# Optimization experiments

Measured on AMD Instinct MI355X. Metric: run time of the kernel, lower is better.

## Reference

```python
import jax, jax.numpy as jnp
import numpy as np

ALPHA = 0.3      # keras LeakyReLU default
BN_EPS = 1e-3    # keras BatchNormalization default
RF, STRIDE = 8, 8


def leaky(x):
    return jnp.where(x >= 0, x, ALPHA * x)


def batchnorm(x, gamma, beta):
    # training-mode BN (train_flag=True): batch statistics over N,H,W
    mean = jnp.mean(x, axis=(0, 1, 2), keepdims=True)
    var = jnp.var(x, axis=(0, 1, 2), keepdims=True)
    return gamma * (x - mean) * jax.lax.rsqrt(var + BN_EPS) + beta


def cbl(x, W, gamma, beta):
    y = jax.lax.conv_general_dilated(x, W, (1, 1), 'SAME',
                                     dimension_numbers=('NHWC', 'HWIO', 'NHWC'))
    return leaky(batchnorm(y, gamma, beta))


def tcbl(x, W, gamma, beta):
    y = jax.lax.conv_transpose(x, W, (2, 2), 'SAME',
                               dimension_numbers=('NHWC', 'HWIO', 'NHWC'))
    return leaky(batchnorm(y, gamma, beta))


def setup_inputs() -> dict:
    key = jax.random.key(0)
    ks = jax.random.split(key, 8)
    B, H, W, C = 8, 128, 128, 128
    nH = (H - RF) // STRIDE + 1
    nW = (W - RF) // STRIDE + 1
    nWin = nH * nW  # 256
    inputs = jax.random.normal(ks[0], (B, H, W, C), dtype=jnp.float32)
    conv_scale = 1.0 / np.sqrt(3 * 3 * C)
    Wq = jax.random.normal(ks[1], (3, 3, C, 128), dtype=jnp.float32) * conv_scale
    Wk = jax.random.normal(ks[2], (3, 3, C, 128), dtype=jnp.float32) * conv_scale
    beta_bias = jax.random.normal(ks[3], (1, 1, 1, nWin), dtype=jnp.float32) * 0.05
    Wt = jax.random.normal(ks[4], (4, 4, nWin, 128), dtype=jnp.float32) / np.sqrt(4 * 4 * nWin)
    return {
        'inputs': inputs,
        'Wq': Wq, 'gq': jnp.ones((128,), jnp.float32), 'bq': jnp.zeros((128,), jnp.float32),
        'Wk': Wk, 'gk': jnp.ones((128,), jnp.float32), 'bk': jnp.zeros((128,), jnp.float32),
        'beta_bias': beta_bias,
        'g1': jnp.ones((nWin,), jnp.float32), 'b1': jnp.zeros((nWin,), jnp.float32),
        'Wt': Wt, 'gt': jnp.ones((128,), jnp.float32), 'bt': jnp.zeros((128,), jnp.float32),
    }


def reference(inputs, Wq, gq, bq, Wk, gk, bk, beta_bias, g1, b1, Wt, gt, bt):
    Q = cbl(inputs, Wq, gq, bq)   # (B,H,W,C)
    K = cbl(inputs, Wk, gk, bk)
    B, H, W, C = Q.shape
    nH = (H - RF) // STRIDE + 1
    nW = (W - RF) // STRIDE + 1
    # window start indices -> (n, RF) gather index grids
    hh = (jnp.arange(nH) * STRIDE)[:, None] + jnp.arange(RF)[None, :]
    ww = (jnp.arange(nW) * STRIDE)[:, None] + jnp.arange(RF)[None, :]

    def patches(x):
        # (B, nH, nW, RF, RF, C) -> (B, nWin, RF*RF*C)
        p = x[:, hh[:, None, :, None], ww[None, :, None, :], :]
        return p.reshape(B, nH * nW, RF * RF * C)

    Qp = patches(Q)
    Kp = patches(K)
    # sim[b, f, q] = <K window f, Q window q>; collapses the 4-nested loop
    sim = jnp.einsum('bfd,bqd->bfq', Kp, Qp).reshape(B, nH, nW, nH * nW)
    sim = sim + beta_bias
    act = leaky(batchnorm(sim, g1, b1))
    return tcbl(act, Wt, gt, bt)  # (B, 2*nH, 2*nW, 128)
```

## Files before the change

### kernel.cpp

```cpp
#include <hip/hip_runtime.h>

typedef __attribute__((ext_vector_type(8))) short bf16x8;
typedef __attribute__((ext_vector_type(8))) unsigned short u16x8;
typedef __attribute__((ext_vector_type(4))) float f32x4;

__device__ __forceinline__ unsigned short f2b(float x) {
    unsigned int u = __float_as_uint(x);
    u += 0x7FFFu + ((u >> 16) & 1u);
    return (unsigned short)(u >> 16);
}
__device__ __forceinline__ float b2f(unsigned short h) {
    return __uint_as_float(((unsigned int)h) << 16);
}
__device__ __forceinline__ float lrelu(float v) { return v >= 0.f ? v : 0.3f * v; }

#define GLL(gp, lp) __builtin_amdgcn_global_load_lds( \
    (const __attribute__((address_space(1))) unsigned int*)(gp), \
    (__attribute__((address_space(3))) unsigned int*)(lp), 16, 0, 0)


__global__ __launch_bounds__(256) void k0a_prep(
        const float* __restrict__ Wq, const float* __restrict__ Wk,
        const float* __restrict__ Wt, unsigned short* __restrict__ WqT,
        unsigned short* __restrict__ WkT, unsigned short* __restrict__ WtT,
        float* __restrict__ S) {
    int idx = blockIdx.x * 256 + threadIdx.x;
    int gs = gridDim.x * 256;
    for (int i = idx; i < 2048; i += gs) S[i] = 0.f;
    for (int i = idx; i < 147456; i += gs) {
        int tap = i >> 14, r = i & 16383, ci = r >> 7, co = r & 127;
        int ch = ci >> 6, e = ci & 63;
        int dst = ((tap * 2 + ch) * 128 + co) * 64 + (((e >> 3) ^ (co & 7)) << 3) + (e & 7);
        WqT[dst] = f2b(Wq[i]);
        WkT[dst] = f2b(Wk[i]);
    }
    for (int i = idx; i < 524288; i += gs) {
        int t = i >> 15, r = i & 32767, ci = r >> 7, co = r & 127;
        WtT[(((size_t)t << 7) + co) * 256 + ci] = f2b(Wt[i]);
    }
}

__global__ __launch_bounds__(256) void k0b_padx(const float* __restrict__ X,
                                                unsigned short* __restrict__ Xb) {
    int c = blockIdx.x * 256 + threadIdx.x;
    int k8 = c & 7;
    int t = c >> 3;
    int wp = t % 130; t /= 130;
    int ch = t & 1; t >>= 1;
    int hp = t % 130; int b = t / 130;
    u16x8 o;
    if (hp >= 1 && hp <= 128 && wp >= 1 && wp <= 128) {
        const float* s = X + (((size_t)(b * 128 + hp - 1) * 128) + (wp - 1)) * 128 + ch * 64 + k8 * 8;
        float4 f0 = *(const float4*)(s);
        float4 f1 = *(const float4*)(s + 4);
        o[0] = f2b(f0.x); o[1] = f2b(f0.y); o[2] = f2b(f0.z); o[3] = f2b(f0.w);
        o[4] = f2b(f1.x); o[5] = f2b(f1.y); o[6] = f2b(f1.z); o[7] = f2b(f1.w);
    } else {
#pragma unroll
        for (int j = 0; j < 8; ++j) o[j] = 0;
    }
    *(u16x8*)&Xb[(size_t)c * 8] = o;
}

__global__ __launch_bounds__(512, 4) void k1_conv(
        const unsigned short* __restrict__ Xb,
        const unsigned short* __restrict__ WqT, const unsigned short* __restrict__ WkT,
        unsigned short* __restrict__ Qraw, unsigned short* __restrict__ Kraw,
        float* __restrict__ S) {
    __shared__ unsigned short s_row[2 * 130 * 72];
    __shared__ unsigned short s_w[2][128 * 64];
    __shared__ float s_st[256];
    const int tid = threadIdx.x;
    const int x = blockIdx.x;
    const int xcd = x & 7, sdec = x >> 3;
    const int b = sdec >> 4, r16 = sdec & 15;
    const int hp = xcd * 8 + (r16 >> 1), conv = r16 & 1;
    const int h0 = hp * 2;
    const int lane = tid & 63, wv = tid >> 6;
    const int wm = wv & 3, wn = wv >> 2;
    const int l15 = lane & 15, kof = (lane >> 4) * 8;
    const int ar = wm >> 1;
    const int awb = (wm & 1) * 64;
    const int nb = wn * 64;

    const unsigned short* W = conv ? WkT : WqT;
    const int gofs = wv * 2048 + lane * 16;

    f32x4 acc[4][4];
#pragma unroll
    for (int i = 0; i < 4; ++i)
#pragma unroll
        for (int j = 0; j < 4; ++j) acc[i][j] = (f32x4){0.f, 0.f, 0.f, 0.f};
    if (tid < 256) s_st[tid] = 0.f;

    {
        const char* src = (const char*)W;
        char* dst = (char*)&s_w[0][0] + wv * 2048;
        GLL(src + gofs, dst);
        GLL(src + gofs + 1024, dst + 1024);
    }

#pragma unroll
    for (int ch = 0; ch < 2; ++ch) {
#pragma unroll
        for (int dy = 0; dy < 3; ++dy) {
#pragma unroll
            for (int dx = 0; dx < 3; ++dx) {
                const int p = (ch * 3 + dy) * 3 + dx;
                __builtin_amdgcn_s_barrier();
                if (dx == 0) {
                    const unsigned short* src0 = Xb + (size_t)((b * 130 + h0 + dy) * 2 + ch) * 8320;
                    const unsigned short* src1 = Xb + (size_t)((b * 130 + h0 + dy + 1) * 2 + ch) * 8320;
                    for (int c = tid; c < 2080; c += 512) {
                        int r = (c >= 1040);
                        int cw = r ? c - 1040 : c;
                        int w = cw >> 3, k8 = cw & 7;
                        *(u16x8*)&s_row[(r * 130 + w) * 72 + k8 * 8] =
                            *(const u16x8*)&((r ? src1 : src0)[cw * 8]);
                    }
                }
                if (p < 17) {
                    const int pn = p + 1;
                    const int nch = pn / 9, ntap = pn % 9;
                    const char* src = (const char*)(W + ((size_t)(ntap * 2 + nch) << 13));
                    char* dst = (char*)&s_w[pn & 1][0] + wv * 2048;
                    GLL(src + gofs, dst);
                    GLL(src + gofs + 1024, dst + 1024);
                    asm volatile("s_waitcnt vmcnt(2) lgkmcnt(0)" ::: "memory");
                } else {
                    asm volatile("s_waitcnt vmcnt(0) lgkmcnt(0)" ::: "memory");
                }
                __builtin_amdgcn_sched_barrier(0);
                __builtin_amdgcn_s_barrier();
                const unsigned short* wb = &s_w[p & 1][0];
#pragma unroll
                for (int kc = 0; kc < 2; ++kc) {
                    const int ci = kc * 32 + kof;
                    bf16x8 a[4], bb[4];
#pragma unroll
                    for (int mf = 0; mf < 4; ++mf)
                        a[mf] = *(const bf16x8*)&s_row[(ar * 130 + awb + mf * 16 + l15 + dx) * 72 + ci];
#pragma unroll
                    for (int nf = 0; nf < 4; ++nf) {
                        int co = nb + nf * 16 + l15;
                        bb[nf] = *(const bf16x8*)&wb[co * 64 + (((ci >> 3) ^ (co & 7)) << 3)];
                    }
#pragma unroll
                    for (int mf = 0; mf < 4; ++mf)
#pragma unroll
                        for (int nf = 0; nf < 4; ++nf)
                            acc[mf][nf] = __builtin_amdgcn_mfma_f32_16x16x32_bf16(
                                a[mf], bb[nf], acc[mf][nf], 0, 0, 0);
                }
            }
        }
    }
    __syncthreads();
    unsigned short* obase = conv ? Kraw : Qraw;
    const int h = h0 + ar;
    float sl[4] = {0.f, 0.f, 0.f, 0.f}, ssl[4] = {0.f, 0.f, 0.f, 0.f};
#pragma unroll
    for (int mf = 0; mf < 4; ++mf)
#pragma unroll
        for (int nf = 0; nf < 4; ++nf)
#pragma unroll
            for (int r = 0; r < 4; ++r) {
                float v = acc[mf][nf][r];
                int w = awb + mf * 16 + (lane >> 4) * 4 + r;
                int co = nb + nf * 16 + l15;
                obase[((size_t)(b * 128 + h) * 128 + w) * 128 + co] = f2b(v);
                sl[nf] += v; ssl[nf] += v * v;
            }
#pragma unroll
    for (int nf = 0; nf < 4; ++nf) {
        float s = sl[nf], ss = ssl[nf];
        s += __shfl_xor(s, 16); s += __shfl_xor(s, 32);
        ss += __shfl_xor(ss, 16); ss += __shfl_xor(ss, 32);
        if (lane < 16) {
            int chn = nb + nf * 16 + lane;
            atomicAdd(&s_st[chn], s);
            atomicAdd(&s_st[128 + chn], ss);
        }
    }
    __syncthreads();
    if (tid < 256) {
        int dst = (tid < 128) ? (conv * 128 + tid) : (256 + conv * 128 + (tid - 128));
        atomicAdd(&S[dst], s_st[tid]);
    }
}

__global__ __launch_bounds__(512, 2) void k3_sim(const unsigned short* __restrict__ Qp,
                                                 const unsigned short* __restrict__ Kp,
                                                 const float* __restrict__ S,
                                                 const float* __restrict__ gq, const float* __restrict__ bq,
                                                 const float* __restrict__ gk, const float* __restrict__ bk,
                                                 float* __restrict__ part) {
    __shared__ unsigned short sA[128 * 136];
    __shared__ unsigned short sB[128 * 136];
    __shared__ float s_p[512];
    const int tid = threadIdx.x;
    const int x = blockIdx.x;
    const int kc = x & 7, sdec = x >> 3;
    const int b = sdec >> 2, mn = sdec & 3;
    const int mi = mn >> 1, ni = mn & 1;
    const int lane = tid & 63, wv = tid >> 6;
    const int wm = wv & 1, wn = wv >> 1;
    if (tid < 256) {
        const float inv_n = 1.f / 131072.f;
        float mean = S[tid] * inv_n;
        float var = S[256 + tid] * inv_n - mean * mean;
        float g  = (tid < 128) ? gq[tid] : gk[tid - 128];
        float be = (tid < 128) ? bq[tid] : bk[tid - 128];
        float sc = g * rsqrtf(var + 1e-3f);
        s_p[tid] = sc;
        s_p[256 + tid] = be - mean * sc;
    }
    f32x4 acc[4][2];
#pragma unroll
    for (int i = 0; i < 4; ++i)
#pragma unroll
        for (int j = 0; j < 2; ++j) acc[i][j] = (f32x4){0.f, 0.f, 0.f, 0.f};
    const int kof = (lane >> 4) * 8;
    const int arow = wm * 64 + (lane & 15);
    const int brow = wn * 32 + (lane & 15);

    for (int s = 0; s < 8; ++s) {
        const int py = kc, px = s;
        __syncthreads();
        for (int c = tid; c < 2048; c += 512) {
            int r = c >> 4, k8 = c & 15;
            int cb = k8 * 8;
            int f = mi * 128 + r;
            size_t sa = ((size_t)(b * 128 + ((f >> 4) * 8 + py)) * 128 + ((f & 15) * 8 + px)) * 128 + cb;
            int q = ni * 128 + r;
            size_t sb = ((size_t)(b * 128 + ((q >> 4) * 8 + py)) * 128 + ((q & 15) * 8 + px)) * 128 + cb;
            u16x8 va = *(const u16x8*)&Kp[sa];
            u16x8 vb = *(const u16x8*)&Qp[sb];
            u16x8 oa, ob;
#pragma unroll
            for (int j = 0; j < 8; ++j) {
                float fk = b2f(va[j]);
                fk = lrelu(s_p[128 + cb + j] * fk + s_p[384 + cb + j]);
                oa[j] = f2b(fk);
                float fq = b2f(vb[j]);
                fq = lrelu(s_p[cb + j] * fq + s_p[256 + cb + j]);
                ob[j] = f2b(fq);
            }
            *(u16x8*)&sA[r * 136 + cb] = oa;
            *(u16x8*)&sB[r * 136 + cb] = ob;
        }
        __syncthreads();
#pragma unroll
        for (int k4 = 0; k4 < 4; ++k4) {
            const int ci = k4 * 32 + kof;
            bf16x8 a[4], bb[2];
#pragma unroll
            for (int mf = 0; mf < 4; ++mf)
                a[mf] = *(const bf16x8*)&sA[(arow + mf * 16) * 136 + ci];
#pragma unroll
            for (int nf = 0; nf < 2; ++nf)
                bb[nf] = *(const bf16x8*)&sB[(brow + nf * 16) * 136 + ci];
#pragma unroll
            for (int mf = 0; mf < 4; ++mf)
#pragma unroll
                for (int nf = 0; nf < 2; ++nf)
                    acc[mf][nf] = __builtin_amdgcn_mfma_f32_16x16x32_bf16(
                        a[mf], bb[nf], acc[mf][nf], 0, 0, 0);
        }
    }
    const size_t base = (size_t)(kc * 8 + b) * 65536;
#pragma unroll
    for (int mf = 0; mf < 4; ++mf)
#pragma unroll
        for (int nf = 0; nf < 2; ++nf)
#pragma unroll
            for (int r = 0; r < 4; ++r) {
                int f = mi * 128 + wm * 64 + mf * 16 + (lane >> 4) * 4 + r;
                int q = ni * 128 + wn * 32 + nf * 16 + (lane & 15);
                part[base + (size_t)f * 256 + q] = acc[mf][nf][r];
            }
}

__global__ __launch_bounds__(256) void k4_red(const float* __restrict__ part,
                                              const float* __restrict__ beta,
                                              float* __restrict__ sim, float* __restrict__ S) {
    int row0 = blockIdx.x * 8;
    int q = threadIdx.x;
    float bsum = 0.f, bss = 0.f;
    float bb = beta[q];
    for (int rr = 0; rr < 8; ++rr) {
        int row = row0 + rr;
        float s = 0.f;
#pragma unroll
        for (int kcc = 0; kcc < 8; ++kcc)
            s += part[(size_t)kcc * 524288 + (size_t)row * 256 + q];
        s += bb;
        sim[(size_t)row * 256 + q] = s;
        bsum += s; bss += s * s;
    }
    atomicAdd(&S[512 + q], bsum);
    atomicAdd(&S[768 + q], bss);
}

__global__ __launch_bounds__(256) void k5b_act(const float* __restrict__ sim,
                                               const float* __restrict__ S,
                                               const float* __restrict__ g1, const float* __restrict__ b1,
                                               unsigned short* __restrict__ actp) {
    __shared__ float s_p[512];
    {
        int c = threadIdx.x;
        const float inv_n = 1.f / 2048.f;
        float mean = S[512 + c] * inv_n;
        float var = S[768 + c] * inv_n - mean * mean;
        float sc = g1[c] * rsqrtf(var + 1e-3f);
        s_p[c] = sc;
        s_p[256 + c] = b1[c] - mean * sc;
    }
    __syncthreads();
    int c = blockIdx.x * 256 + threadIdx.x;
    if (c >= 186624) return;
    int k8 = c & 31;
    int t = c >> 5;
    int jp = t % 18; t /= 18;
    int ip = t % 18; int b = t / 18;
    u16x8 o;
    if (ip >= 1 && ip <= 16 && jp >= 1 && jp <= 16) {
        int f = (ip - 1) * 16 + (jp - 1);
        const float* s = sim + (size_t)(b * 256 + f) * 256 + k8 * 8;
#pragma unroll
        for (int j = 0; j < 8; ++j) {
            int ci = k8 * 8 + j;
            o[j] = f2b(lrelu(s_p[ci] * s[j] + s_p[256 + ci]));
        }
    } else {
#pragma unroll
        for (int j = 0; j < 8; ++j) o[j] = 0;
    }
    *(u16x8*)&actp[(size_t)c * 8] = o;
}

__global__ __launch_bounds__(512, 2) void k6_tconv(const unsigned short* __restrict__ actp,
                                                   const unsigned short* __restrict__ WtT,
                                                   float* __restrict__ y, float* __restrict__ S) {
    __shared__ unsigned short sA[64 * 264];
    __shared__ unsigned short sB[128 * 264];
    const int tid = threadIdx.x;
    const int x = blockIdx.x;
    const int iq = x & 3, pw = (x >> 2) & 1, ph = (x >> 3) & 1, b = x >> 4;
    const int lane = tid & 63, wv = tid >> 6;
    f32x4 acc[4];
#pragma unroll
    for (int i = 0; i < 4; ++i) acc[i] = (f32x4){0.f, 0.f, 0.f, 0.f};
    const int kof = (lane >> 4) * 8;
    const int arow = lane & 15;
    const int bco = wv * 16 + (lane & 15);

    for (int a2 = 0; a2 < 2; ++a2)
        for (int c2 = 0; c2 < 2; ++c2) {
            const int kh = ph + 2 * a2, kw = pw + 2 * c2;
            __syncthreads();
            for (int c = tid; c < 2048; c += 512) {
                int r = c >> 5, k8 = c & 31;
                int i = iq * 4 + (r >> 4), j = r & 15;
                size_t sa = (size_t)((b * 18 + (i + a2 + ph)) * 18 + (j + c2 + pw)) * 256 + k8 * 8;
                *(u16x8*)&sA[r * 264 + k8 * 8] = *(const u16x8*)&actp[sa];
            }
            for (int c = tid; c < 4096; c += 512) {
                int co = c >> 5, k8 = c & 31;
                size_t sb = (size_t)((kh * 4 + kw) * 128 + co) * 256 + k8 * 8;
                *(u16x8*)&sB[co * 264 + k8 * 8] = *(const u16x8*)&WtT[sb];
            }
            __syncthreads();
#pragma unroll
            for (int k8c = 0; k8c < 8; ++k8c) {
                const int ci = k8c * 32 + kof;
                bf16x8 bb = *(const bf16x8*)&sB[bco * 264 + ci];
#pragma unroll
                for (int mf = 0; mf < 4; ++mf) {
                    bf16x8 a = *(const bf16x8*)&sA[(arow + mf * 16) * 264 + ci];
                    acc[mf] = __builtin_amdgcn_mfma_f32_16x16x32_bf16(a, bb, acc[mf], 0, 0, 0);
                }
            }
        }
    float sl = 0.f, ssl = 0.f;
#pragma unroll
    for (int mf = 0; mf < 4; ++mf)
#pragma unroll
        for (int r = 0; r < 4; ++r) {
            float v = acc[mf][r];
            int m = mf * 16 + (lane >> 4) * 4 + r;
            int i = iq * 4 + (m >> 4), j = m & 15;
            int oh = 2 * i + ph, ow = 2 * j + pw;
            y[(size_t)((b * 32 + oh) * 32 + ow) * 128 + bco] = v;
            sl += v; ssl += v * v;
        }
    sl += __shfl_xor(sl, 16); sl += __shfl_xor(sl, 32);
    ssl += __shfl_xor(ssl, 16); ssl += __shfl_xor(ssl, 32);
    if (lane < 16) {
        atomicAdd(&S[1024 + wv * 16 + lane], sl);
        atomicAdd(&S[1152 + wv * 16 + lane], ssl);
    }
}

__global__ __launch_bounds__(256) void k8_out(const float* __restrict__ y,
                                              const float* __restrict__ S,
                                              const float* __restrict__ gt, const float* __restrict__ bt,
                                              float* __restrict__ out) {
    __shared__ float s_p[256];
    if (threadIdx.x < 128) {
        int c = threadIdx.x;
        const float inv_n = 1.f / 8192.f;
        float mean = S[1024 + c] * inv_n;
        float var = S[1152 + c] * inv_n - mean * mean;
        float sc = gt[c] * rsqrtf(var + 1e-3f);
        s_p[c] = sc;
        s_p[128 + c] = bt[c] - mean * sc;
    }
    __syncthreads();
    int c = blockIdx.x * 256 + threadIdx.x;
    const float4 v = *(const float4*)&y[(size_t)c * 4];
    int cb = (c & 31) * 4;
    float4 o;
    o.x = lrelu(s_p[cb + 0] * v.x + s_p[128 + cb + 0]);
    o.y = lrelu(s_p[cb + 1] * v.y + s_p[128 + cb + 1]);
    o.z = lrelu(s_p[cb + 2] * v.z + s_p[128 + cb + 2]);
    o.w = lrelu(s_p[cb + 3] * v.w + s_p[128 + cb + 3]);
    *(float4*)&out[(size_t)c * 4] = o;
}

extern "C" void kernel_launch(void* const* d_in, const int* in_sizes, int n_in,
                              void* d_out, int out_size, void* d_ws, size_t ws_size,
                              hipStream_t stream) {
    (void)in_sizes; (void)n_in; (void)out_size; (void)ws_size;
    const float* X    = (const float*)d_in[0];
    const float* Wq   = (const float*)d_in[1];
    const float* gq   = (const float*)d_in[2];
    const float* bq   = (const float*)d_in[3];
    const float* Wk   = (const float*)d_in[4];
    const float* gk   = (const float*)d_in[5];
    const float* bk   = (const float*)d_in[6];
    const float* beta = (const float*)d_in[7];
    const float* g1   = (const float*)d_in[8];
    const float* b1   = (const float*)d_in[9];
    const float* Wt   = (const float*)d_in[10];
    const float* gt   = (const float*)d_in[11];
    const float* bt   = (const float*)d_in[12];

    char* ws = (char*)d_ws;
    unsigned short* Qraw = (unsigned short*)(ws + 0ull);
    unsigned short* Kraw = (unsigned short*)(ws + 33554432ull);
    unsigned short* WqT  = (unsigned short*)(ws + 67108864ull);
    unsigned short* WkT  = (unsigned short*)(ws + 67403776ull);
    unsigned short* WtT  = (unsigned short*)(ws + 67698688ull);
    float* S             = (float*)(ws + 68747264ull);
    unsigned short* Xb   = (unsigned short*)(ws + 68761600ull);
    float* part          = (float*)(ws + 68761600ull);
    float* sim           = (float*)(ws + 0ull);
    unsigned short* actp = (unsigned short*)(ws + 4194304ull);
    float* y             = (float*)(ws + 8388608ull);
    float* out           = (float*)d_out;

    k0a_prep<<<1024, 256, 0, stream>>>(Wq, Wk, Wt, WqT, WkT, WtT, S);
    k0b_padx<<<8450, 256, 0, stream>>>(X, Xb);
    k1_conv<<<1024, 512, 0, stream>>>(Xb, WqT, WkT, Qraw, Kraw, S);
    k3_sim<<<256, 512, 0, stream>>>(Qraw, Kraw, S, gq, bq, gk, bk, part);
    k4_red<<<256, 256, 0, stream>>>(part, beta, sim, S);
    k5b_act<<<729, 256, 0, stream>>>(sim, S, g1, b1, actp);
    k6_tconv<<<128, 512, 0, stream>>>(actp, WtT, y, S);
    k8_out<<<1024, 256, 0, stream>>>(y, S, gt, bt, out);
}
```

Before: 170.4 us.

## Replace conv BN-stat atomics with partials and finalize kernel; split tconv finer

Each conv block now writes its per-channel sum and sum-of-squares to its own slot in a partial buffer instead of doing global atomicAdds into shared BN counters. A new single-block kernel reduces those partials and computes the BN scale and shift once. The sim kernel then just loads the precomputed scale and shift. Separately, the transposed-conv kernel halves its M tile so it launches twice as many blocks (256 instead of 128) to fill more CUs, and the outer ch/dy conv loops are no longer force-unrolled. This trades atomic contention for an extra launch and a serial 512-step reduction, and trades per-block data reuse for parallelism in the tconv.

Result: slower. 184.6 us (+8.3%).

```diff
diff --git a/kernel.cpp b/kernel.cpp
--- a/kernel.cpp
+++ b/kernel.cpp
@@ -66,7 +66,7 @@
         const unsigned short* __restrict__ Xb,
         const unsigned short* __restrict__ WqT, const unsigned short* __restrict__ WkT,
         unsigned short* __restrict__ Qraw, unsigned short* __restrict__ Kraw,
-        float* __restrict__ S) {
+        float* __restrict__ Spart) {
     __shared__ unsigned short s_row[2 * 130 * 72];
     __shared__ unsigned short s_w[2][128 * 64];
     __shared__ float s_st[256];
@@ -100,9 +100,7 @@
         GLL(src + gofs + 1024, dst + 1024);
     }
 
-#pragma unroll
     for (int ch = 0; ch < 2; ++ch) {
-#pragma unroll
         for (int dy = 0; dy < 3; ++dy) {
 #pragma unroll
             for (int dx = 0; dx < 3; ++dx) {
@@ -184,16 +182,34 @@
     }
     __syncthreads();
     if (tid < 256) {
-        int dst = (tid < 128) ? (conv * 128 + tid) : (256 + conv * 128 + (tid - 128));
-        atomicAdd(&S[dst], s_st[tid]);
-    }
+        Spart[((size_t)conv * 512 + (b * 64 + hp)) * 256 + tid] = s_st[tid];
+    }
+}
+
+__global__ void k2a_fin(const float* __restrict__ gq, const float* __restrict__ bq,
+                        const float* __restrict__ gk, const float* __restrict__ bk,
+                        const float* __restrict__ Spart, float* __restrict__ S) {
+    int c = threadIdx.x;
+    int conv = c >> 7, co = c & 127;
+    const float* base = Spart + (size_t)conv * 512 * 256;
+    float s = 0.f, ss = 0.f;
+    for (int i = 0; i < 512; ++i) {
+        s  += base[i * 256 + co];
+        ss += base[i * 256 + 128 + co];
+    }
+    const float inv_n = 1.f / 131072.f;
+    float mean = s * inv_n;
+    float var = ss * inv_n - mean * mean;
+    float g  = conv ? gk[co] : gq[co];
+    float be = conv ? bk[co] : bq[co];
+    float sc = g * rsqrtf(var + 1e-3f);
+    S[c] = sc;
+    S[256 + c] = be - mean * sc;
 }
 
 __global__ __launch_bounds__(512, 2) void k3_sim(const unsigned short* __restrict__ Qp,
                                                  const unsigned short* __restrict__ Kp,
-                                                 const float* __restrict__ S,
-                                                 const float* __restrict__ gq, const float* __restrict__ bq,
-                                                 const float* __restrict__ gk, const float* __restrict__ bk,
+                                                 const float* __restrict__ P,
                                                  float* __restrict__ part) {
     __shared__ unsigned short sA[128 * 136];
     __shared__ unsigned short sB[128 * 136];
@@ -205,16 +221,7 @@
     const int mi = mn >> 1, ni = mn & 1;
     const int lane = tid & 63, wv = tid >> 6;
     const int wm = wv & 1, wn = wv >> 1;
-    if (tid < 256) {
-        const float inv_n = 1.f / 131072.f;
-        float mean = S[tid] * inv_n;
-        float var = S[256 + tid] * inv_n - mean * mean;
-        float g  = (tid < 128) ? gq[tid] : gk[tid - 128];
-        float be = (tid < 128) ? bq[tid] : bk[tid - 128];
-        float sc = g * rsqrtf(var + 1e-3f);
-        s_p[tid] = sc;
-        s_p[256 + tid] = be - mean * sc;
-    }
+    if (tid < 512) s_p[tid] = P[tid];
     f32x4 acc[4][2];
 #pragma unroll
     for (int i = 0; i < 4; ++i)
@@ -342,15 +349,15 @@
 __global__ __launch_bounds__(512, 2) void k6_tconv(const unsigned short* __restrict__ actp,
                                                    const unsigned short* __restrict__ WtT,
                                                    float* __restrict__ y, float* __restrict__ S) {
-    __shared__ unsigned short sA[64 * 264];
+    __shared__ unsigned short sA[32 * 264];
     __shared__ unsigned short sB[128 * 264];
     const int tid = threadIdx.x;
     const int x = blockIdx.x;
-    const int iq = x & 3, pw = (x >> 2) & 1, ph = (x >> 3) & 1, b = x >> 4;
+    const int iq = x & 7, pw = (x >> 3) & 1, ph = (x >> 4) & 1, b = x >> 5;
     const int lane = tid & 63, wv = tid >> 6;
-    f32x4 acc[4];
-#pragma unroll
-    for (int i = 0; i < 4; ++i) acc[i] = (f32x4){0.f, 0.f, 0.f, 0.f};
+    f32x4 acc[2];
+#pragma unroll
+    for (int i = 0; i < 2; ++i) acc[i] = (f32x4){0.f, 0.f, 0.f, 0.f};
     const int kof = (lane >> 4) * 8;
     const int arow = lane & 15;
     const int bco = wv * 16 + (lane & 15);
@@ -359,9 +366,9 @@
         for (int c2 = 0; c2 < 2; ++c2) {
             const int kh = ph + 2 * a2, kw = pw + 2 * c2;
             __syncthreads();
-            for (int c = tid; c < 2048; c += 512) {
+            for (int c = tid; c < 1024; c += 512) {
                 int r = c >> 5, k8 = c & 31;
-                int i = iq * 4 + (r >> 4), j = r & 15;
+                int i = iq * 2 + (r >> 4), j = r & 15;
                 size_t sa = (size_t)((b * 18 + (i + a2 + ph)) * 18 + (j + c2 + pw)) * 256 + k8 * 8;
                 *(u16x8*)&sA[r * 264 + k8 * 8] = *(const u16x8*)&actp[sa];
             }
@@ -376,7 +383,7 @@
                 const int ci = k8c * 32 + kof;
                 bf16x8 bb = *(const bf16x8*)&sB[bco * 264 + ci];
 #pragma unroll
-                for (int mf = 0; mf < 4; ++mf) {
+                for (int mf = 0; mf < 2; ++mf) {
                     bf16x8 a = *(const bf16x8*)&sA[(arow + mf * 16) * 264 + ci];
                     acc[mf] = __builtin_amdgcn_mfma_f32_16x16x32_bf16(a, bb, acc[mf], 0, 0, 0);
                 }
@@ -384,12 +391,12 @@
         }
     float sl = 0.f, ssl = 0.f;
 #pragma unroll
-    for (int mf = 0; mf < 4; ++mf)
+    for (int mf = 0; mf < 2; ++mf)
 #pragma unroll
         for (int r = 0; r < 4; ++r) {
             float v = acc[mf][r];
             int m = mf * 16 + (lane >> 4) * 4 + r;
-            int i = iq * 4 + (m >> 4), j = m & 15;
+            int i = iq * 2 + (m >> 4), j = m & 15;
             int oh = 2 * i + ph, ow = 2 * j + pw;
             y[(size_t)((b * 32 + oh) * 32 + ow) * 128 + bco] = v;
             sl += v; ssl += v * v;
@@ -455,6 +462,7 @@
     float* S             = (float*)(ws + 68747264ull);
     unsigned short* Xb   = (unsigned short*)(ws + 68761600ull);
     float* part          = (float*)(ws + 68761600ull);
+    float* Spart         = (float*)(ws + 103372800ull);
     float* sim           = (float*)(ws + 0ull);
     unsigned short* actp = (unsigned short*)(ws + 4194304ull);
     float* y             = (float*)(ws + 8388608ull);
@@ -462,10 +470,11 @@
 
     k0a_prep<<<1024, 256, 0, stream>>>(Wq, Wk, Wt, WqT, WkT, WtT, S);
     k0b_padx<<<8450, 256, 0, stream>>>(X, Xb);
-    k1_conv<<<1024, 512, 0, stream>>>(Xb, WqT, WkT, Qraw, Kraw, S);
-    k3_sim<<<256, 512, 0, stream>>>(Qraw, Kraw, S, gq, bq, gk, bk, part);
+    k1_conv<<<1024, 512, 0, stream>>>(Xb, WqT, WkT, Qraw, Kraw, Spart);
+    k2a_fin<<<1, 256, 0, stream>>>(gq, bq, gk, bk, Spart, S);
+    k3_sim<<<256, 512, 0, stream>>>(Qraw, Kraw, S, part);
     k4_red<<<256, 256, 0, stream>>>(part, beta, sim, S);
     k5b_act<<<729, 256, 0, stream>>>(sim, S, g1, b1, actp);
-    k6_tconv<<<128, 512, 0, stream>>>(actp, WtT, y, S);
+    k6_tconv<<<256, 512, 0, stream>>>(actp, WtT, y, S);
     k8_out<<<1024, 256, 0, stream>>>(y, S, gt, bt, out);
 }
```
